# Optimization experiments

Hardware: AMD Instinct MI355X
Metric: run time of the kernel (lower is better)

Reference implementation:

```python
import jax
jax.config.update("jax_enable_x64", True)
import jax.numpy as jnp
import numpy as np

INPUT_DIM = 2048
NUM_BINS = 32
RMS_EPS = 1e-4  # RunningMeanStd initial count


def setup_inputs() -> dict:
    key = jax.random.key(0)
    k1, k2 = jax.random.split(key)
    features = jax.random.normal(k1, (64, 256, INPUT_DIM), dtype=jnp.float32)
    # register_buffer: randn(input_dim, num_bins) / sqrt(input_dim)
    random_projection = jax.random.normal(k2, (INPUT_DIM, NUM_BINS), dtype=jnp.float32) / np.sqrt(INPUT_DIM)
    return {"features": features, "random_projection": random_projection}


def _occurrence_counts(keys):
    """For each element, 1 + number of earlier elements with the same key.
    Stable argsort keeps original order inside each duplicate run, so the
    rank within a run equals the sequential visit count."""
    n = keys.shape[0]
    order = jnp.argsort(keys)  # stable
    sk = keys[order]
    idx = jnp.arange(n, dtype=jnp.int64)
    new_run = jnp.concatenate([jnp.ones((1,), bool), sk[1:] != sk[:-1]])
    starts = jax.lax.cummax(jnp.where(new_run, idx, 0))
    counts_sorted = idx - starts + 1
    return jnp.zeros(n, jnp.int64).at[order].set(counts_sorted)


def reference(features, random_projection):
    batch, seq, feat = features.shape
    x = features.reshape(-1, feat)
    n = x.shape[0]

    # RunningMeanStd.update from fresh state (mean=0, var=1, count=1e-4)
    bm = jnp.mean(x, axis=0)
    bv = jnp.var(x, axis=0, ddof=1)  # torch .var(dim=0) is unbiased
    tot = RMS_EPS + n
    mean = bm * (n / tot)  # delta = bm - 0
    m2 = 1.0 * RMS_EPS + bv * n + (bm ** 2) * (RMS_EPS * n / tot)
    var = m2 / tot
    sigma = jnp.sqrt(var + 1e-8)

    normalized = (x - mean) / sigma
    projected = normalized @ random_projection  # [n, num_bins]
    bits = (projected > 0).astype(jnp.int64)
    powers = (2 ** jnp.arange(min(NUM_BINS, 63), dtype=jnp.int64))
    h = (bits[:, : powers.shape[0]] * powers).sum(axis=-1)  # < 2^32

    env = jnp.arange(n, dtype=jnp.int64) % batch  # default env_indices path
    keys = h * batch + env  # unique per (env, hash), fits int64
    counts = _occurrence_counts(keys)

    rewards = 1.0 / jnp.sqrt(counts.astype(features.dtype))
    return rewards.reshape(batch, seq, 1)
```

## Files before the change

### kernel.cpp

```cpp
#include <hip/hip_runtime.h>
#include <math.h>

#define FEAT 2048
#define NBINS 32
#define NROWS 16384
#define NCLS 64
#define SB 256
#define RPB 64

typedef __attribute__((ext_vector_type(8))) short short8;
typedef __attribute__((ext_vector_type(4))) float f32x4;

static __device__ __forceinline__ unsigned int pk2bf(float a, float b) {
    unsigned ua = __float_as_uint(a);
    unsigned ub = __float_as_uint(b);
    ua = (ua + 0x7FFFu + ((ua >> 16) & 1u)) >> 16;
    ub = (ub + 0x7FFFu + ((ub >> 16) & 1u)) & 0xFFFF0000u;
    return ua | ub;
}

__global__ __launch_bounds__(256) void k1_stats(const float* __restrict__ x,
                                                float* __restrict__ pS1,
                                                float* __restrict__ pS2,
                                                unsigned int* __restrict__ xbf) {
    const int b = blockIdx.x, t = threadIdx.x;
    const float4* xb = reinterpret_cast<const float4*>(x) + (size_t)b * RPB * (FEAT / 4);
    const int k0a = 4 * t;
    const int k0b = 4 * t + 1024;
    const int cpA = ((k0a >> 7) * 4 + ((k0a >> 5) & 3)) * 1024 + (((k0a >> 3) & 3) << 8) + ((k0a & 7) << 1);
    const int cpB = ((k0b >> 7) * 4 + ((k0b >> 5) & 3)) * 1024 + (((k0b >> 3) & 3) << 8) + ((k0b & 7) << 1);
    char* tile = reinterpret_cast<char*>(xbf) + (size_t)b * 262144;

    float4 s1a = make_float4(0.f,0.f,0.f,0.f), s1b = make_float4(0.f,0.f,0.f,0.f);
    float4 s2a = make_float4(0.f,0.f,0.f,0.f), s2b = make_float4(0.f,0.f,0.f,0.f);
    for (int r = 0; r < RPB; ++r) {
        const float4 va = xb[(size_t)r * (FEAT / 4) + t];
        const float4 vb = xb[(size_t)r * (FEAT / 4) + t + 256];
        s1a.x += va.x; s1a.y += va.y; s1a.z += va.z; s1a.w += va.w;
        s2a.x += va.x * va.x; s2a.y += va.y * va.y; s2a.z += va.z * va.z; s2a.w += va.w * va.w;
        s1b.x += vb.x; s1b.y += vb.y; s1b.z += vb.z; s1b.w += vb.w;
        s2b.x += vb.x * vb.x; s2b.y += vb.y * vb.y; s2b.z += vb.z * vb.z; s2b.w += vb.w * vb.w;
        const int rp = (r >> 4) * 65536 + (r & 15) * 16;
        uint2 pa, pb;
        pa.x = pk2bf(va.x, va.y); pa.y = pk2bf(va.z, va.w);
        pb.x = pk2bf(vb.x, vb.y); pb.y = pk2bf(vb.z, vb.w);
        *reinterpret_cast<uint2*>(tile + cpA + rp) = pa;
        *reinterpret_cast<uint2*>(tile + cpB + rp) = pb;
    }
    float4* o1 = reinterpret_cast<float4*>(pS1 + (size_t)b * FEAT);
    float4* o2 = reinterpret_cast<float4*>(pS2 + (size_t)b * FEAT);
    o1[t] = s1a; o1[t + 256] = s1b;
    o2[t] = s2a; o2[t + 256] = s2b;
}

__global__ __launch_bounds__(256) void k2_final(const float* __restrict__ pS1,
                                                const float* __restrict__ pS2,
                                                const float* __restrict__ P,
                                                float* __restrict__ ms,
                                                unsigned int* __restrict__ QTf) {
    __shared__ double sh1[8][32];
    __shared__ double sh2[8][32];
    __shared__ float isig_sh[32];
    const int t = threadIdx.x;
    const int ci = t & 31, seg = t >> 5;
    const int c = blockIdx.x * 32 + ci;
    double S1 = 0.0, S2 = 0.0;
    for (int i = 0; i < 32; ++i) {
        const int k = seg * 32 + i;
        S1 += (double)pS1[(size_t)k * FEAT + c];
        S2 += (double)pS2[(size_t)k * FEAT + c];
    }
    sh1[seg][ci] = S1; sh2[seg][ci] = S2;
    __syncthreads();
    if (t < 32) {
        double s1 = 0.0, s2 = 0.0;
        #pragma unroll
        for (int s = 0; s < 8; ++s) { s1 += sh1[s][t]; s2 += sh2[s][t]; }
        const int cc = blockIdx.x * 32 + t;
        const double n = (double)NROWS;
        const double bm = s1 / n;
        const double bv = (s2 - s1 * s1 / n) / (n - 1.0);
        const double tot = 1e-4 + n;
        const double mean = bm * (n / tot);
        const double m2 = 1e-4 + bv * n + bm * bm * (1e-4 * n / tot);
        const double var = m2 / tot;
        const double isig = 1.0 / sqrt(var + 1e-8);
        ms[cc] = (float)(mean * isig);
        isig_sh[t] = (float)isig;
    }
    __syncthreads();
    const int nb = t >> 7;
    const int lane = (t & 127) >> 1;
    const int half = t & 1;
    const int lrow = lane & 15, lk = lane >> 4;
    const int bin = nb * 16 + lrow;
    const int ccl = lk * 8 + half * 4;
    const int cc = blockIdx.x * 32 + ccl;
    unsigned int w0 = pk2bf(P[(size_t)cc * NBINS + bin] * isig_sh[ccl],
                            P[(size_t)(cc + 1) * NBINS + bin] * isig_sh[ccl + 1]);
    unsigned int w1 = pk2bf(P[(size_t)(cc + 2) * NBINS + bin] * isig_sh[ccl + 2],
                            P[(size_t)(cc + 3) * NBINS + bin] * isig_sh[ccl + 3]);
    const int ch = blockIdx.x >> 2, ks = blockIdx.x & 3;
    char* dst = reinterpret_cast<char*>(QTf) +
                (size_t)(((nb * 16 + ch) * 4 + ks) * 1024 + lane * 16 + half * 8);
    uint2 pk; pk.x = w0; pk.y = w1;
    *reinterpret_cast<uint2*>(dst) = pk;
}

__global__ __launch_bounds__(256) void k2b_offset(const float* __restrict__ ms,
                                                  const float* __restrict__ P,
                                                  float* __restrict__ offs) {
    __shared__ double sh[256];
    const int b = blockIdx.x, t = threadIdx.x;
    double s = 0.0;
    for (int f = t; f < FEAT; f += 256) s += (double)ms[f] * (double)P[(size_t)f * NBINS + b];
    sh[t] = s;
    __syncthreads();
    for (int st = 128; st > 0; st >>= 1) {
        if (t < st) sh[t] += sh[t + st];
        __syncthreads();
    }
    if (t == 0) offs[b] = (float)sh[0];
}

__global__ __launch_bounds__(256) void k3_mfma(const unsigned int* __restrict__ xbf,
                                               const unsigned int* __restrict__ QTf,
                                               const float* __restrict__ offs,
                                               unsigned int* __restrict__ hout) {
    const int t = threadIdx.x;
    const int w = t >> 6, l = t & 63;
    const int lrow = l & 15, lk = l >> 4;
    const int bid = blockIdx.x;

    const short8* ap  = reinterpret_cast<const short8*>(xbf) + (size_t)bid * 16384 + w * 4096 + l;
    const short8* b0p = reinterpret_cast<const short8*>(QTf) + l;
    const short8* b1p = b0p + 4096;

    f32x4 acc0 = {0.f, 0.f, 0.f, 0.f};
    f32x4 acc1 = {0.f, 0.f, 0.f, 0.f};

    #pragma unroll 8
    for (int ss = 0; ss < 64; ++ss) {
        const short8 a  = ap[ss * 64];
        const short8 b0 = b0p[ss * 64];
        const short8 b1 = b1p[ss * 64];
        acc0 = __builtin_amdgcn_mfma_f32_16x16x32_bf16(a, b0, acc0, 0, 0, 0);
        acc1 = __builtin_amdgcn_mfma_f32_16x16x32_bf16(a, b1, acc1, 0, 0, 0);
    }

    const float o0 = offs[lrow];
    const float o1 = offs[16 + lrow];
    #pragma unroll
    for (int r = 0; r < 4; ++r) {
        const unsigned long long m0 = __ballot(acc0[r] > o0);
        const unsigned long long m1 = __ballot(acc1[r] > o1);
        if (lrow == 0) {
            const unsigned int h =
                (unsigned int)((m0 >> (16 * lk)) & 0xFFFFull) |
                ((unsigned int)((m1 >> (16 * lk)) & 0xFFFFull) << 16);
            const int irow = w * 16 + lk * 4 + r;
            hout[(size_t)irow * 256 + bid] = h;
        }
    }
}

__global__ __launch_bounds__(256) void k4_count(const unsigned int* __restrict__ hcls,
                                                float* __restrict__ out) {
    __shared__ unsigned int hh[256];
    const int c = blockIdx.x, t = threadIdx.x;
    hh[t] = hcls[(size_t)c * 256 + t];
    __syncthreads();
    const unsigned int mine = hh[t];
    int cnt = 1;
    for (int j = 0; j < 256; ++j) {
        cnt += (j < t && hh[j] == mine) ? 1 : 0;
    }
    out[(size_t)t * NCLS + c] = 1.0f / sqrtf((float)cnt);
}

extern "C" void kernel_launch(void* const* d_in, const int* in_sizes, int n_in,
                              void* d_out, int out_size, void* d_ws, size_t ws_size,
                              hipStream_t stream) {
    const float* x = (const float*)d_in[0];
    const float* P = (const float*)d_in[1];
    float* out = (float*)d_out;
    char* ws = (char*)d_ws;

    float* pS1 = (float*)(ws);
    float* pS2 = (float*)(ws + (size_t)SB * FEAT * 4);
    float* ms  = (float*)(ws + (size_t)2 * SB * FEAT * 4);
    float* offsB = ms + FEAT;
    unsigned int* xbf = (unsigned int*)(ws + (size_t)8 * 1024 * 1024);
    unsigned int* QTf = (unsigned int*)(ws + (size_t)8 * 1024 * 1024 + (size_t)64 * 1024 * 1024);
    unsigned int* h   = (unsigned int*)(ws + (size_t)8 * 1024 * 1024 + (size_t)64 * 1024 * 1024 + 131072);

    k1_stats<<<SB, 256, 0, stream>>>(x, pS1, pS2, xbf);
    k2_final<<<64, 256, 0, stream>>>(pS1, pS2, P, ms, QTf);
    k2b_offset<<<32, 256, 0, stream>>>(ms, P, offsB);
    k3_mfma<<<256, 256, 0, stream>>>(xbf, QTf, offsB, h);
    k4_count<<<NCLS, 256, 0, stream>>>(h, out);
}
```

Measured before the change: 70.34 us.

## Drop bf16 staging copy; convert fp32 input to bf16 inside MFMA kernel

The stats kernel no longer writes a swizzled bf16 copy of the 128MB input. The MFMA kernel now reads the fp32 features directly and packs them to bf16 in registers. This removes 64MB of writes and 64MB of reads but adds a second 128MB fp32 read of the input in k3. The stats kernel is also split into 1024 blocks of 16 rows, fully unrolled, for more parallelism, and the finalisation loop is adjusted to match. k3's direct row-strided fp32 loads may coalesce less well than the prior tiled layout.

```diff
diff --git a/kernel.cpp b/kernel.cpp
--- a/kernel.cpp
+++ b/kernel.cpp
@@ -5,8 +5,8 @@
 #define NBINS 32
 #define NROWS 16384
 #define NCLS 64
-#define SB 256
-#define RPB 64
+#define SB 1024
+#define RPB 16
 
 typedef __attribute__((ext_vector_type(8))) short short8;
 typedef __attribute__((ext_vector_type(4))) float f32x4;
@@ -21,18 +21,12 @@
 
 __global__ __launch_bounds__(256) void k1_stats(const float* __restrict__ x,
                                                 float* __restrict__ pS1,
-                                                float* __restrict__ pS2,
-                                                unsigned int* __restrict__ xbf) {
+                                                float* __restrict__ pS2) {
     const int b = blockIdx.x, t = threadIdx.x;
     const float4* xb = reinterpret_cast<const float4*>(x) + (size_t)b * RPB * (FEAT / 4);
-    const int k0a = 4 * t;
-    const int k0b = 4 * t + 1024;
-    const int cpA = ((k0a >> 7) * 4 + ((k0a >> 5) & 3)) * 1024 + (((k0a >> 3) & 3) << 8) + ((k0a & 7) << 1);
-    const int cpB = ((k0b >> 7) * 4 + ((k0b >> 5) & 3)) * 1024 + (((k0b >> 3) & 3) << 8) + ((k0b & 7) << 1);
-    char* tile = reinterpret_cast<char*>(xbf) + (size_t)b * 262144;
-
     float4 s1a = make_float4(0.f,0.f,0.f,0.f), s1b = make_float4(0.f,0.f,0.f,0.f);
     float4 s2a = make_float4(0.f,0.f,0.f,0.f), s2b = make_float4(0.f,0.f,0.f,0.f);
+    #pragma unroll
     for (int r = 0; r < RPB; ++r) {
         const float4 va = xb[(size_t)r * (FEAT / 4) + t];
         const float4 vb = xb[(size_t)r * (FEAT / 4) + t + 256];
@@ -40,12 +34,6 @@
         s2a.x += va.x * va.x; s2a.y += va.y * va.y; s2a.z += va.z * va.z; s2a.w += va.w * va.w;
         s1b.x += vb.x; s1b.y += vb.y; s1b.z += vb.z; s1b.w += vb.w;
         s2b.x += vb.x * vb.x; s2b.y += vb.y * vb.y; s2b.z += vb.z * vb.z; s2b.w += vb.w * vb.w;
-        const int rp = (r >> 4) * 65536 + (r & 15) * 16;
-        uint2 pa, pb;
-        pa.x = pk2bf(va.x, va.y); pa.y = pk2bf(va.z, va.w);
-        pb.x = pk2bf(vb.x, vb.y); pb.y = pk2bf(vb.z, vb.w);
-        *reinterpret_cast<uint2*>(tile + cpA + rp) = pa;
-        *reinterpret_cast<uint2*>(tile + cpB + rp) = pb;
     }
     float4* o1 = reinterpret_cast<float4*>(pS1 + (size_t)b * FEAT);
     float4* o2 = reinterpret_cast<float4*>(pS2 + (size_t)b * FEAT);
@@ -64,9 +52,10 @@
     const int t = threadIdx.x;
     const int ci = t & 31, seg = t >> 5;
     const int c = blockIdx.x * 32 + ci;
+    const int segN = SB >> 3;
     double S1 = 0.0, S2 = 0.0;
-    for (int i = 0; i < 32; ++i) {
-        const int k = seg * 32 + i;
+    for (int i = 0; i < segN; ++i) {
+        const int k = seg * segN + i;
         S1 += (double)pS1[(size_t)k * FEAT + c];
         S2 += (double)pS2[(size_t)k * FEAT + c];
     }
@@ -123,7 +112,7 @@
     if (t == 0) offs[b] = (float)sh[0];
 }
 
-__global__ __launch_bounds__(256) void k3_mfma(const unsigned int* __restrict__ xbf,
+__global__ __launch_bounds__(256) void k3_mfma(const float* __restrict__ x,
                                                const unsigned int* __restrict__ QTf,
                                                const float* __restrict__ offs,
                                                unsigned int* __restrict__ hout) {
@@ -132,7 +121,7 @@
     const int lrow = l & 15, lk = l >> 4;
     const int bid = blockIdx.x;
 
-    const short8* ap  = reinterpret_cast<const short8*>(xbf) + (size_t)bid * 16384 + w * 4096 + l;
+    const float* ax = x + (size_t)(bid * 64 + w * 16 + lrow) * FEAT + lk * 8;
     const short8* b0p = reinterpret_cast<const short8*>(QTf) + l;
     const short8* b1p = b0p + 4096;
 
@@ -141,7 +130,12 @@
 
     #pragma unroll 8
     for (int ss = 0; ss < 64; ++ss) {
-        const short8 a  = ap[ss * 64];
+        const float4 va = *reinterpret_cast<const float4*>(ax + ss * 32);
+        const float4 vb = *reinterpret_cast<const float4*>(ax + ss * 32 + 4);
+        uint4 ap;
+        ap.x = pk2bf(va.x, va.y); ap.y = pk2bf(va.z, va.w);
+        ap.z = pk2bf(vb.x, vb.y); ap.w = pk2bf(vb.z, vb.w);
+        const short8 a  = __builtin_bit_cast(short8, ap);
         const short8 b0 = b0p[ss * 64];
         const short8 b1 = b1p[ss * 64];
         acc0 = __builtin_amdgcn_mfma_f32_16x16x32_bf16(a, b0, acc0, 0, 0, 0);
@@ -188,15 +182,14 @@
 
     float* pS1 = (float*)(ws);
     float* pS2 = (float*)(ws + (size_t)SB * FEAT * 4);
-    float* ms  = (float*)(ws + (size_t)2 * SB * FEAT * 4);
+    float* ms  = (float*)(ws + (size_t)16 * 1024 * 1024);
     float* offsB = ms + FEAT;
-    unsigned int* xbf = (unsigned int*)(ws + (size_t)8 * 1024 * 1024);
-    unsigned int* QTf = (unsigned int*)(ws + (size_t)8 * 1024 * 1024 + (size_t)64 * 1024 * 1024);
-    unsigned int* h   = (unsigned int*)(ws + (size_t)8 * 1024 * 1024 + (size_t)64 * 1024 * 1024 + 131072);
+    unsigned int* QTf = (unsigned int*)(ws + (size_t)17 * 1024 * 1024);
+    unsigned int* h   = (unsigned int*)(ws + (size_t)18 * 1024 * 1024);
 
-    k1_stats<<<SB, 256, 0, stream>>>(x, pS1, pS2, xbf);
+    k1_stats<<<SB, 256, 0, stream>>>(x, pS1, pS2);
     k2_final<<<64, 256, 0, stream>>>(pS1, pS2, P, ms, QTf);
     k2b_offset<<<32, 256, 0, stream>>>(ms, P, offsB);
-    k3_mfma<<<256, 256, 0, stream>>>(xbf, QTf, offsB, h);
+    k3_mfma<<<256, 256, 0, stream>>>(x, QTf, offsB, h);
     k4_count<<<NCLS, 256, 0, stream>>>(h, out);
 }
```

After: 74.93 us. 1.07x slower.
